# Performance work log

Measured on AMD Instinct MI355X. Metric: run time of the kernel, lower is better.

The kernel has to match this reference:

```python
import jax, jax.numpy as jnp
import numpy as np

B, N, D = 2, 2048, 1024
H = 16
HD = D // H  # 64
SCALE = 8.0 / HD  # muP scale = 0.125
EPS = 1e-5


def setup_inputs() -> dict:
    key = jax.random.key(0)
    ks = jax.random.split(key, 7)
    s = 0.02  # realistic init scale for weights
    return {
        "xq": jax.random.normal(ks[0], (B, N, D), jnp.float32),
        "xk": jax.random.normal(ks[1], (B, N, D), jnp.float32),
        "xv": jax.random.normal(ks[2], (B, N, D), jnp.float32),
        "wq": jax.random.normal(ks[3], (D, D), jnp.float32) * s,
        "wk": jax.random.normal(ks[4], (D, D), jnp.float32) * s,
        "wv": jax.random.normal(ks[5], (D, D), jnp.float32) * s,
        "wproj": jax.random.normal(ks[6], (D, D), jnp.float32) * s,
    }


def _layernorm_noaffine(x):
    # Fp32LayerNorm over last dim, no bias / no affine params
    x32 = x.astype(jnp.float32)
    mu = jnp.mean(x32, axis=-1, keepdims=True)
    var = jnp.mean(jnp.square(x32 - mu), axis=-1, keepdims=True)
    return ((x32 - mu) * jax.lax.rsqrt(var + EPS)).astype(x.dtype)


def _heads(x):
    # [B, N, H*HD] -> [B, H, N, HD]
    b, n, _ = x.shape
    return x.reshape(b, n, H, HD).transpose(0, 2, 1, 3)


def reference(xq, xk, xv, wq, wk, wv, wproj):
    # nn.Linear: y = x @ W^T (no bias)
    q = _heads(xq @ wq.T)
    k = _heads(xk @ wk.T)
    v = _heads(xv @ wv.T)
    q = _layernorm_noaffine(q)
    k = _layernorm_noaffine(k)
    # dense attention (score_mod=None, block_mask=None), muP scale
    scores = jnp.einsum("bhqd,bhkd->bhqk", q, k) * SCALE
    attn = jax.nn.softmax(scores, axis=-1)
    o = jnp.einsum("bhqk,bhkd->bhqd", attn, v)
    o = o.transpose(0, 2, 1, 3).reshape(xq.shape[0], xq.shape[1], D)
    return o @ wproj.T
```

## Files before the change

### kernel.cpp

```cpp
#include <hip/hip_runtime.h>

typedef __bf16 bf16x8 __attribute__((ext_vector_type(8)));
typedef float f32x4 __attribute__((ext_vector_type(4)));
typedef float f32x16 __attribute__((ext_vector_type(16)));
typedef unsigned u32x4 __attribute__((ext_vector_type(4)));

#define DEV __device__ __forceinline__
#define L2E 1.44269504f

DEV unsigned short f2bf(float f) {
  unsigned u = __float_as_uint(f);
  u += 0x7fffu + ((u >> 16) & 1u);
  return (unsigned short)(u >> 16);
}
DEV float bf2f(unsigned short h) { return __uint_as_float(((unsigned)h) << 16); }

DEV void gload16(const void* g, void* l) {
  __builtin_amdgcn_global_load_lds((const __attribute__((address_space(1))) void*)g,
                                   (__attribute__((address_space(3))) void*)l, 16, 0, 0);
}

DEV unsigned cvtpk2(float lo, float hi) {
  unsigned r;
  asm("v_cvt_pk_bf16_f32 %0, %1, %2" : "=v"(r) : "v"(lo), "v"(hi));
  return r;
}
DEV void plswap(unsigned& a, unsigned& b) {
  asm volatile("v_permlane32_swap_b32 %0, %1" : "+v"(a), "+v"(b));
}
DEV float ex2(float x) {
  float r;
  asm("v_exp_f32 %0, %1" : "=v"(r) : "v"(x));
  return r;
}
DEV float max3(float a, float b, float c) {
  float r;
  asm("v_max3_f32 %0, %1, %2, %3" : "=v"(r) : "v"(a), "v"(b), "v"(c));
  return r;
}


__global__ __launch_bounds__(256) void cvt7(const float* xq, const float* xk, const float* xv,
                                            const float* wq, const float* wk, const float* wv,
                                            const float* wp, ushort4* xqb, ushort4* xkb,
                                            ushort4* xvb, ushort4* wqb, ushort4* wkb,
                                            ushort4* wvb, ushort4* wpb, int nx4, int nw4) {
  const int y = blockIdx.y;
  const float4* s;
  ushort4* d;
  int n;
  switch (y) {
    case 0: s = (const float4*)xq; d = xqb; n = nx4; break;
    case 1: s = (const float4*)xk; d = xkb; n = nx4; break;
    case 2: s = (const float4*)xv; d = xvb; n = nx4; break;
    case 3: s = (const float4*)wq; d = wqb; n = nw4; break;
    case 4: s = (const float4*)wk; d = wkb; n = nw4; break;
    case 5: s = (const float4*)wv; d = wvb; n = nw4; break;
    default: s = (const float4*)wp; d = wpb; n = nw4; break;
  }
  for (int i = blockIdx.x * 256 + threadIdx.x; i < n; i += gridDim.x * 256) {
    float4 v = s[i];
    ushort4 o;
    o.x = f2bf(v.x); o.y = f2bf(v.y); o.z = f2bf(v.z); o.w = f2bf(v.w);
    d[i] = o;
  }
}

template <bool SWAP>
DEV void gemm_core(const unsigned short* __restrict__ A, const unsigned short* __restrict__ W,
                   char* sA, char* sB, f32x4 acc[4][4], int bm, int bn, int tid) {
  const int w = tid >> 6, lane = tid & 63;
  const int wm = w >> 1, wn = w & 1;
  const char* aB = (const char*)A + ((size_t)(bm * 128 + (lane >> 3)) << 11) +
                   (((lane & 7) ^ (lane >> 3)) << 4);
  const char* bB = (const char*)W + ((size_t)(bn * 128 + (lane >> 3)) << 11) +
                   (((lane & 7) ^ (lane >> 3)) << 4);
  const int ldsBase = w * 1024;

  for (int kt = 0; kt < 16; ++kt) {
    const int ko = kt * 128;
#pragma unroll
    for (int c = 0; c < 4; ++c) {
      gload16(aB + ((size_t)(c * 32 + w * 8) << 11) + ko, sA + c * 4096 + ldsBase);
      gload16(bB + ((size_t)(c * 32 + w * 8) << 11) + ko, sB + c * 4096 + ldsBase);
    }
    __syncthreads();
#pragma unroll
    for (int kk = 0; kk < 2; ++kk) {
      const int ch = ((kk * 4 + (lane >> 4)) ^ (lane & 7)) << 4;
      bf16x8 aF[4], bF[4];
#pragma unroll
      for (int mi = 0; mi < 4; ++mi)
        aF[mi] = *(const bf16x8*)(sA + (wm * 64 + mi * 16 + (lane & 15)) * 128 + ch);
#pragma unroll
      for (int ni = 0; ni < 4; ++ni)
        bF[ni] = *(const bf16x8*)(sB + (wn * 64 + ni * 16 + (lane & 15)) * 128 + ch);
#pragma unroll
      for (int mi = 0; mi < 4; ++mi)
#pragma unroll
        for (int ni = 0; ni < 4; ++ni)
          acc[mi][ni] = SWAP ? __builtin_amdgcn_mfma_f32_16x16x32_bf16(bF[ni], aF[mi],
                                                                       acc[mi][ni], 0, 0, 0)
                             : __builtin_amdgcn_mfma_f32_16x16x32_bf16(aF[mi], bF[ni],
                                                                       acc[mi][ni], 0, 0, 0);
    }
    __syncthreads();
  }
}

__global__ __launch_bounds__(256, 3) void gemm_qkv(
    const unsigned short* __restrict__ xq, const unsigned short* __restrict__ xk,
    const unsigned short* __restrict__ xv, const unsigned short* __restrict__ wq,
    const unsigned short* __restrict__ wk, const unsigned short* __restrict__ wv,
    unsigned short* __restrict__ qh, unsigned short* __restrict__ kh,
    unsigned short* __restrict__ vt) {
  __shared__ char sA[16384], sB[16384];
  const int z = blockIdx.z;
  const int flat = blockIdx.x + (blockIdx.y << 3);
  const int xcd = flat & 7, ii = flat >> 3;
  const int bm = xcd * 4 + (ii >> 3), bn = ii & 7;
  const int tid = threadIdx.x, w = tid >> 6, lane = tid & 63;
  const int wm = w >> 1, wn = w & 1;

  if (z == 2) {
    f32x4 acc[4][4];
#pragma unroll
    for (int i = 0; i < 4; ++i)
#pragma unroll
      for (int j = 0; j < 4; ++j) acc[i][j] = (f32x4){0.f, 0.f, 0.f, 0.f};
    gemm_core<false>(xv, wv, sA, sB, acc, bm, bn, tid);
    const int hb = bn * 2 + wn;
    const int d = (lane & 15);
    const int g0 = bm * 128 + wm * 64 + ((lane >> 4) << 2);
#pragma unroll
    for (int mi = 0; mi < 4; ++mi) {
      const int g = g0 + mi * 16;
      const int b = g >> 11, n0 = g & 2047, tq = n0 >> 6, nn = n0 & 63;
#pragma unroll
      for (int ni = 0; ni < 4; ++ni) {
        const int dd = d + ni * 16;
        char* dst = (char*)vt + ((size_t)((b * 16 + hb) * 32 + tq) << 13) +
                    (((nn >> 4) * 2 + (dd >> 5)) << 10) + (((nn >> 3) & 1) << 9) +
                    ((dd & 31) << 4) + ((nn & 7) << 1);
        *(uint2*)dst = make_uint2(cvtpk2(acc[mi][ni][0], acc[mi][ni][1]),
                                  cvtpk2(acc[mi][ni][2], acc[mi][ni][3]));
      }
    }
  } else {
    const unsigned short* A = z == 0 ? xq : xk;
    const unsigned short* W = z == 0 ? wq : wk;
    f32x4 acc[4][4];
#pragma unroll
    for (int i = 0; i < 4; ++i)
#pragma unroll
      for (int j = 0; j < 4; ++j) acc[i][j] = (f32x4){0.f, 0.f, 0.f, 0.f};
    gemm_core<true>(A, W, sA, sB, acc, bm, bn, tid);
    unsigned short* dst = z == 0 ? qh : kh;
    const float osc = z == 0 ? 0.125f * L2E : 1.0f;
    const int h = bn * 2 + wn;
    const int hiK = lane >> 5;
    const int low8 = ((lane >> 4) & 1) << 3;
#pragma unroll
    for (int mi = 0; mi < 4; ++mi) {
      float s = 0.f, ss = 0.f;
#pragma unroll
      for (int ni = 0; ni < 4; ++ni)
#pragma unroll
        for (int r = 0; r < 4; ++r) {
          const float v = acc[mi][ni][r];
          s += v;
          ss += v * v;
        }
      s += __shfl_xor(s, 16); ss += __shfl_xor(ss, 16);
      s += __shfl_xor(s, 32); ss += __shfl_xor(ss, 32);
      const float mean = s * 0.015625f;
      const float var = ss * 0.015625f - mean * mean;
      const float rstd = rsqrtf(var + 1e-5f) * osc;
      const float mr = mean * rstd;
      const int g = bm * 128 + wm * 64 + mi * 16 + (lane & 15);
      const int b = g >> 11, n = g & 2047;
      const int bh = b * 16 + h, tq = n >> 6, rr = n & 63;
      char* tbase = (char*)dst + ((size_t)(bh * 32 + tq) << 13);
#pragma unroll
      for (int ni = 0; ni < 4; ++ni) {
        const unsigned u0 = cvtpk2(fmaf(acc[mi][ni][0], rstd, -mr), fmaf(acc[mi][ni][1], rstd, -mr));
        const unsigned u1 = cvtpk2(fmaf(acc[mi][ni][2], rstd, -mr), fmaf(acc[mi][ni][3], rstd, -mr));
        char* p = tbase + ((ni * 2 + (rr >> 5)) << 10) + (hiK << 9) + ((rr & 31) << 4) + low8;
        *(uint2*)p = make_uint2(u0, u1);
      }
    }
  }
}

__global__ __launch_bounds__(256, 3) void gemm_out(const unsigned short* __restrict__ A,
                                                   const unsigned short* __restrict__ Wp,
                                                   float* __restrict__ C) {
  __shared__ char sA[16384], sB[8192];
  const int flat = blockIdx.x + (blockIdx.y << 4);
  const int xcd = flat & 7, ii = flat >> 3;
  const int bm = xcd * 4 + (ii & 3), bn = ii >> 2;
  const int tid = threadIdx.x, w = tid >> 6, lane = tid & 63;
  const int wm = w >> 1, wn = w & 1;
  f32x4 acc[4][2];
#pragma unroll
  for (int i = 0; i < 4; ++i)
#pragma unroll
    for (int j = 0; j < 2; ++j) acc[i][j] = (f32x4){0.f, 0.f, 0.f, 0.f};

  const char* aB = (const char*)A + ((size_t)(bm * 128 + (lane >> 3)) << 11) +
                   (((lane & 7) ^ (lane >> 3)) << 4);
  const char* bB = (const char*)Wp + ((size_t)(bn * 64 + (lane >> 3)) << 11) +
                   (((lane & 7) ^ (lane >> 3)) << 4);
  const int ldsBase = w * 1024;
  for (int kt = 0; kt < 16; ++kt) {
    const int ko = kt * 128;
#pragma unroll
    for (int c = 0; c < 4; ++c)
      gload16(aB + ((size_t)(c * 32 + w * 8) << 11) + ko, sA + c * 4096 + ldsBase);
#pragma unroll
    for (int c = 0; c < 2; ++c)
      gload16(bB + ((size_t)(c * 32 + w * 8) << 11) + ko, sB + c * 4096 + ldsBase);
    __syncthreads();
#pragma unroll
    for (int kk = 0; kk < 2; ++kk) {
      const int ch = ((kk * 4 + (lane >> 4)) ^ (lane & 7)) << 4;
      bf16x8 aF[4], bF[2];
#pragma unroll
      for (int mi = 0; mi < 4; ++mi)
        aF[mi] = *(const bf16x8*)(sA + (wm * 64 + mi * 16 + (lane & 15)) * 128 + ch);
#pragma unroll
      for (int ni = 0; ni < 2; ++ni)
        bF[ni] = *(const bf16x8*)(sB + (wn * 32 + ni * 16 + (lane & 15)) * 128 + ch);
#pragma unroll
      for (int mi = 0; mi < 4; ++mi)
#pragma unroll
        for (int ni = 0; ni < 2; ++ni)
          acc[mi][ni] = __builtin_amdgcn_mfma_f32_16x16x32_bf16(bF[ni], aF[mi], acc[mi][ni], 0, 0, 0);
    }
    __syncthreads();
  }
  const int m0 = bm * 128 + wm * 64 + (lane & 15);
  const int nb = bn * 64 + wn * 32 + ((lane >> 4) << 2);
#pragma unroll
  for (int mi = 0; mi < 4; ++mi)
#pragma unroll
    for (int ni = 0; ni < 2; ++ni) {
      const f32x4 v = acc[mi][ni];
      *(float4*)&C[(size_t)(m0 + mi * 16) * 1024 + nb + ni * 16] =
          make_float4(v[0], v[1], v[2], v[3]);
    }
}

__global__ __launch_bounds__(256, 4) void attn_fused(
    const unsigned short* __restrict__ Qp, const unsigned short* __restrict__ Kp,
    const unsigned short* __restrict__ Vp, unsigned short* __restrict__ Opart,
    float2* __restrict__ ML) {
  const int bid = blockIdx.x;
  const int xcd = bid & 7, idx = bid >> 3;
  const int bh = ((idx & 3) << 3) | xcd;
  const int rest = idx >> 2;
  const int half = rest & 1;
  const int qt = rest >> 1;
  __shared__ char smem[32768];
  const int tid = threadIdx.x, w = tid >> 6, lane = tid & 63;
  const int q5 = lane & 31, hi = lane >> 5;

  const char* qg = (const char*)Qp + ((size_t)(bh * 32 + qt * 2) << 13);
  const char* kg = (const char*)Kp + ((size_t)(bh * 32 + half * 16) << 13);
  const char* vg = (const char*)Vp + ((size_t)(bh * 32 + half * 16) << 13);

#pragma unroll
  for (int t = 0; t < 4; ++t)
    gload16(qg + (w * 4 + t) * 1024 + lane * 16, smem + (w * 4 + t) * 1024);
  __syncthreads();
  bf16x8 qf[4];
  {
    const int qbase = (w >> 1) * 8192 + ((w & 1) << 10);
#pragma unroll
    for (int dc = 0; dc < 4; ++dc)
      qf[dc] = *(const bf16x8*)(smem + qbase + (dc << 11) + lane * 16);
  }
  __syncthreads();

#pragma unroll
  for (int t = 0; t < 2; ++t) {
    gload16(kg + (w * 2 + t) * 1024 + lane * 16, smem + (w * 2 + t) * 1024);
    gload16(vg + (w * 2 + t) * 1024 + lane * 16, smem + 16384 + (w * 2 + t) * 1024);
  }

  const u32x4 onesw = {0x3F803F80u, 0x3F803F80u, 0x3F803F80u, 0x3F803F80u};
  const bf16x8 ones = __builtin_bit_cast(bf16x8, onesw);

  f32x16 o0 = {0,0,0,0,0,0,0,0,0,0,0,0,0,0,0,0};
  f32x16 o1 = {0,0,0,0,0,0,0,0,0,0,0,0,0,0,0,0};
  f32x16 lacc = {0,0,0,0,0,0,0,0,0,0,0,0,0,0,0,0};
  float m = -1e30f;

  for (int kt = 0; kt < 16; ++kt) {
    const int cur = kt & 1;
    const int kOff = cur * 8192;
    const int vOff = 16384 + cur * 8192;
    __syncthreads();
    if (kt < 15) {
      const int kN = (cur ^ 1) * 8192, vN = 16384 + (cur ^ 1) * 8192;
#pragma unroll
      for (int t = 0; t < 2; ++t) {
        gload16(kg + (size_t)(kt + 1) * 8192 + (w * 2 + t) * 1024 + lane * 16,
                smem + kN + (w * 2 + t) * 1024);
        gload16(vg + (size_t)(kt + 1) * 8192 + (w * 2 + t) * 1024 + lane * 16,
                smem + vN + (w * 2 + t) * 1024);
      }
    }
    f32x16 s0 = {0,0,0,0,0,0,0,0,0,0,0,0,0,0,0,0};
    f32x16 s1 = {0,0,0,0,0,0,0,0,0,0,0,0,0,0,0,0};
    __builtin_amdgcn_s_setprio(1);
#pragma unroll
    for (int dc = 0; dc < 4; ++dc) {
      const bf16x8 kf0 = *(const bf16x8*)(smem + kOff + (dc << 11) + lane * 16);
      const bf16x8 kf1 = *(const bf16x8*)(smem + kOff + (dc << 11) + 1024 + lane * 16);
      s0 = __builtin_amdgcn_mfma_f32_32x32x16_bf16(kf0, qf[dc], s0, 0, 0, 0);
      s1 = __builtin_amdgcn_mfma_f32_32x32x16_bf16(kf1, qf[dc], s1, 0, 0, 0);
    }
    __builtin_amdgcn_s_setprio(0);
    float tt[12];
#pragma unroll
    for (int r = 0; r < 10; ++r) {
      const float a = (3 * r) < 16 ? s0[(3 * r) & 15] : s1[(3 * r) & 15];
      const float b = (3 * r + 1) < 16 ? s0[(3 * r + 1) & 15] : s1[(3 * r + 1) & 15];
      const float c = (3 * r + 2) < 16 ? s0[(3 * r + 2) & 15] : s1[(3 * r + 2) & 15];
      tt[r] = max3(a, b, c);
    }
    tt[10] = s1[14]; tt[11] = s1[15];
    tt[0] = max3(tt[0], tt[1], tt[2]);
    tt[1] = max3(tt[3], tt[4], tt[5]);
    tt[2] = max3(tt[6], tt[7], tt[8]);
    tt[3] = max3(tt[9], tt[10], tt[11]);
    const float loc = fmaxf(max3(tt[0], tt[1], tt[2]), tt[3]);
    const float mx = fmaxf(loc, __shfl_xor(loc, 32));
    if (__any(mx > m + 8.f)) {
      const float mn = fmaxf(m, mx);
      const float corr = ex2(m - mn);
      lacc[0] *= corr;
#pragma unroll
      for (int r = 0; r < 16; ++r) { o0[r] *= corr; o1[r] *= corr; }
      m = mn;
    }
    const float nm = -m;
    unsigned pk[4][4];
#define DO_CHUNK(c, SV, B)                                      \
  {                                                             \
    float p0 = ex2(SV[B + 0] + nm);                             \
    float p1 = ex2(SV[B + 1] + nm);                             \
    float p2 = ex2(SV[B + 2] + nm);                             \
    float p3 = ex2(SV[B + 3] + nm);                             \
    float p4 = ex2(SV[B + 4] + nm);                             \
    float p5 = ex2(SV[B + 5] + nm);                             \
    float p6 = ex2(SV[B + 6] + nm);                             \
    float p7 = ex2(SV[B + 7] + nm);                             \
    unsigned a0 = cvtpk2(p0, p1), a1 = cvtpk2(p2, p3);          \
    unsigned b0 = cvtpk2(p4, p5), b1 = cvtpk2(p6, p7);          \
    plswap(a0, b0);                                             \
    plswap(a1, b1);                                             \
    pk[c][0] = a0; pk[c][1] = a1; pk[c][2] = b0; pk[c][3] = b1; \
  }
    DO_CHUNK(0, s0, 0)
    DO_CHUNK(1, s0, 8)
    DO_CHUNK(2, s1, 0)
    DO_CHUNK(3, s1, 8)
#undef DO_CHUNK
    __builtin_amdgcn_s_setprio(1);
#pragma unroll
    for (int kk = 0; kk < 4; ++kk) {
      const bf16x8 vf0 = *(const bf16x8*)(smem + vOff + (kk << 11) + lane * 16);
      const bf16x8 vf1 = *(const bf16x8*)(smem + vOff + (kk << 11) + 1024 + lane * 16);
      const u32x4 pw = {pk[kk][0], pk[kk][1], pk[kk][2], pk[kk][3]};
      const bf16x8 pb = __builtin_bit_cast(bf16x8, pw);
      o0 = __builtin_amdgcn_mfma_f32_32x32x16_bf16(vf0, pb, o0, 0, 0, 0);
      o1 = __builtin_amdgcn_mfma_f32_32x32x16_bf16(vf1, pb, o1, 0, 0, 0);
      lacc = __builtin_amdgcn_mfma_f32_32x32x16_bf16(ones, pb, lacc, 0, 0, 0);
    }
    __builtin_amdgcn_s_setprio(0);
  }

  const float l = lacc[0];
  const float invl = 1.f / l;
  const int q = qt * 128 + w * 32 + q5;
  const size_t prow = (size_t)(half * 32 + bh) * 2048 + q;
  unsigned short* ob = Opart + prow * 64;
#pragma unroll
  for (int g = 0; g < 4; ++g) {
    unsigned d0 = cvtpk2(o0[4 * g + 0] * invl, o0[4 * g + 1] * invl);
    unsigned d1 = cvtpk2(o0[4 * g + 2] * invl, o0[4 * g + 3] * invl);
    *(uint2*)(ob + 8 * g + 4 * hi) = make_uint2(d0, d1);
    unsigned e0 = cvtpk2(o1[4 * g + 0] * invl, o1[4 * g + 1] * invl);
    unsigned e1 = cvtpk2(o1[4 * g + 2] * invl, o1[4 * g + 3] * invl);
    *(uint2*)(ob + 32 + 8 * g + 4 * hi) = make_uint2(e0, e1);
  }
  if (hi == 0) ML[prow] = make_float2(m, l);
}

__global__ __launch_bounds__(256) void attn_merge(const unsigned short* __restrict__ Op,
                                                  const float2* __restrict__ ML,
                                                  unsigned short* __restrict__ O) {
  const int gid = blockIdx.x * 256 + threadIdx.x;
  const int row = gid >> 3, sub = gid & 7;
  float2 ml[2];
  float mm = -1e30f;
#pragma unroll
  for (int p = 0; p < 2; ++p) {
    ml[p] = ML[p * 65536 + row];
    mm = fmaxf(mm, ml[p].x);
  }
  float wgt[2], wsum = 0.f;
#pragma unroll
  for (int p = 0; p < 2; ++p) {
    wgt[p] = ml[p].y * ex2(ml[p].x - mm);
    wsum += wgt[p];
  }
  const float inv = 1.f / wsum;
  float r[8] = {0.f, 0.f, 0.f, 0.f, 0.f, 0.f, 0.f, 0.f};
#pragma unroll
  for (int p = 0; p < 2; ++p) {
    const uint4 a = *(const uint4*)(Op + ((size_t)(p * 65536) + row) * 64 + sub * 8);
    const unsigned av[4] = {a.x, a.y, a.z, a.w};
#pragma unroll
    for (int j = 0; j < 4; ++j) {
      r[2 * j] += wgt[p] * bf2f((unsigned short)(av[j] & 0xffff));
      r[2 * j + 1] += wgt[p] * bf2f((unsigned short)(av[j] >> 16));
    }
  }
  unsigned ov[4];
#pragma unroll
  for (int j = 0; j < 4; ++j)
    ov[j] = cvtpk2(r[2 * j] * inv, r[2 * j + 1] * inv);
  const int bh = row >> 11, q = row & 2047, bb = bh >> 4, h = bh & 15;
  *(uint4*)(O + ((size_t)(bb * 2048 + q) * 1024 + h * 64 + sub * 8)) =
      make_uint4(ov[0], ov[1], ov[2], ov[3]);
}

extern "C" void kernel_launch(void* const* d_in, const int* in_sizes, int n_in,
                              void* d_out, int out_size, void* d_ws, size_t ws_size,
                              hipStream_t stream) {
  const float* xq = (const float*)d_in[0];
  const float* xk = (const float*)d_in[1];
  const float* xv = (const float*)d_in[2];
  const float* wq = (const float*)d_in[3];
  const float* wk = (const float*)d_in[4];
  const float* wv = (const float*)d_in[5];
  const float* wp = (const float*)d_in[6];

  const size_t NX = 4194304;
  const size_t NW = 1048576;
  unsigned short* base = (unsigned short*)d_ws;
  unsigned short* xqb = base;
  unsigned short* xkb = base + NX;
  unsigned short* xvb = base + 2 * NX;
  unsigned short* wqb = base + 3 * NX;
  unsigned short* wkb = wqb + NW;
  unsigned short* wvb = wkb + NW;
  unsigned short* wpb = base + 3 * NX + 4 * NW;
  unsigned short* qh = wpb + NW;
  unsigned short* kh = qh + NX;
  unsigned short* vt = kh + NX;
  unsigned short* obf = vt + NX;
  float2* ml = (float2*)(obf + NX);
  unsigned short* opart = base;

  cvt7<<<dim3(512, 7), 256, 0, stream>>>(xq, xk, xv, wq, wk, wv, wp, (ushort4*)xqb,
                                         (ushort4*)xkb, (ushort4*)xvb, (ushort4*)wqb,
                                         (ushort4*)wkb, (ushort4*)wvb, (ushort4*)wpb,
                                         (int)(NX / 4), (int)(NW / 4));

  gemm_qkv<<<dim3(8, 32, 3), 256, 0, stream>>>(xqb, xkb, xvb, wqb, wkb, wvb, qh, kh, vt);

  attn_fused<<<1024, 256, 0, stream>>>(qh, kh, vt, opart, ml);
  attn_merge<<<2048, 256, 0, stream>>>(opart, ml, obf);

  gemm_out<<<dim3(16, 32), 256, 0, stream>>>(obf, wpb, (float*)d_out);
}
```

Baseline: 122.9 us.

## Triple-buffer K/V tiles in attention with prefetch depth two and vmcnt waits

Moves the attention kernel's K/V shared-memory staging from double to triple buffering. Tiles are prefetched two iterations ahead, and a partial s_waitcnt vmcnt(4) plus a raw barrier replaces the per-iteration __syncthreads. The aim is to hide more global-load latency behind the MFMA work. The cost is 48KB of LDS per block, with launch bounds lowered to 3 blocks per CU, which may reduce occupancy and latency hiding across waves.

```diff
diff --git a/kernel.cpp b/kernel.cpp
--- a/kernel.cpp
+++ b/kernel.cpp
@@ -251,7 +251,7 @@
     }
 }
 
-__global__ __launch_bounds__(256, 4) void attn_fused(
+__global__ __launch_bounds__(256, 3) void attn_fused(
     const unsigned short* __restrict__ Qp, const unsigned short* __restrict__ Kp,
     const unsigned short* __restrict__ Vp, unsigned short* __restrict__ Opart,
     float2* __restrict__ ML) {
@@ -261,7 +261,7 @@
   const int rest = idx >> 2;
   const int half = rest & 1;
   const int qt = rest >> 1;
-  __shared__ char smem[32768];
+  __shared__ char smem[49152];
   const int tid = threadIdx.x, w = tid >> 6, lane = tid & 63;
   const int q5 = lane & 31, hi = lane >> 5;
 
@@ -283,10 +283,14 @@
   __syncthreads();
 
 #pragma unroll
-  for (int t = 0; t < 2; ++t) {
-    gload16(kg + (w * 2 + t) * 1024 + lane * 16, smem + (w * 2 + t) * 1024);
-    gload16(vg + (w * 2 + t) * 1024 + lane * 16, smem + 16384 + (w * 2 + t) * 1024);
-  }
+  for (int tt = 0; tt < 2; ++tt)
+#pragma unroll
+    for (int t = 0; t < 2; ++t) {
+      gload16(kg + (size_t)tt * 8192 + (w * 2 + t) * 1024 + lane * 16,
+              smem + tt * 8192 + (w * 2 + t) * 1024);
+      gload16(vg + (size_t)tt * 8192 + (w * 2 + t) * 1024 + lane * 16,
+              smem + 24576 + tt * 8192 + (w * 2 + t) * 1024);
+    }
 
   const u32x4 onesw = {0x3F803F80u, 0x3F803F80u, 0x3F803F80u, 0x3F803F80u};
   const bf16x8 ones = __builtin_bit_cast(bf16x8, onesw);
@@ -296,57 +300,60 @@
   f32x16 lacc = {0,0,0,0,0,0,0,0,0,0,0,0,0,0,0,0};
   float m = -1e30f;
 
-  for (int kt = 0; kt < 16; ++kt) {
-    const int cur = kt & 1;
-    const int kOff = cur * 8192;
-    const int vOff = 16384 + cur * 8192;
-    __syncthreads();
-    if (kt < 15) {
-      const int kN = (cur ^ 1) * 8192, vN = 16384 + (cur ^ 1) * 8192;
-#pragma unroll
-      for (int t = 0; t < 2; ++t) {
-        gload16(kg + (size_t)(kt + 1) * 8192 + (w * 2 + t) * 1024 + lane * 16,
-                smem + kN + (w * 2 + t) * 1024);
-        gload16(vg + (size_t)(kt + 1) * 8192 + (w * 2 + t) * 1024 + lane * 16,
-                smem + vN + (w * 2 + t) * 1024);
-      }
-    }
-    f32x16 s0 = {0,0,0,0,0,0,0,0,0,0,0,0,0,0,0,0};
-    f32x16 s1 = {0,0,0,0,0,0,0,0,0,0,0,0,0,0,0,0};
-    __builtin_amdgcn_s_setprio(1);
-#pragma unroll
-    for (int dc = 0; dc < 4; ++dc) {
-      const bf16x8 kf0 = *(const bf16x8*)(smem + kOff + (dc << 11) + lane * 16);
-      const bf16x8 kf1 = *(const bf16x8*)(smem + kOff + (dc << 11) + 1024 + lane * 16);
-      s0 = __builtin_amdgcn_mfma_f32_32x32x16_bf16(kf0, qf[dc], s0, 0, 0, 0);
-      s1 = __builtin_amdgcn_mfma_f32_32x32x16_bf16(kf1, qf[dc], s1, 0, 0, 0);
-    }
-    __builtin_amdgcn_s_setprio(0);
-    float tt[12];
-#pragma unroll
-    for (int r = 0; r < 10; ++r) {
-      const float a = (3 * r) < 16 ? s0[(3 * r) & 15] : s1[(3 * r) & 15];
-      const float b = (3 * r + 1) < 16 ? s0[(3 * r + 1) & 15] : s1[(3 * r + 1) & 15];
-      const float c = (3 * r + 2) < 16 ? s0[(3 * r + 2) & 15] : s1[(3 * r + 2) & 15];
-      tt[r] = max3(a, b, c);
-    }
-    tt[10] = s1[14]; tt[11] = s1[15];
-    tt[0] = max3(tt[0], tt[1], tt[2]);
-    tt[1] = max3(tt[3], tt[4], tt[5]);
-    tt[2] = max3(tt[6], tt[7], tt[8]);
-    tt[3] = max3(tt[9], tt[10], tt[11]);
-    const float loc = fmaxf(max3(tt[0], tt[1], tt[2]), tt[3]);
-    const float mx = fmaxf(loc, __shfl_xor(loc, 32));
-    if (__any(mx > m + 8.f)) {
-      const float mn = fmaxf(m, mx);
-      const float corr = ex2(m - mn);
-      lacc[0] *= corr;
-#pragma unroll
-      for (int r = 0; r < 16; ++r) { o0[r] *= corr; o1[r] *= corr; }
-      m = mn;
-    }
-    const float nm = -m;
-    unsigned pk[4][4];
+#define ATTN_TILE(kOff, vOff)                                                     \
+  {                                                                               \
+    f32x16 s0 = {0,0,0,0,0,0,0,0,0,0,0,0,0,0,0,0};                                \
+    f32x16 s1 = {0,0,0,0,0,0,0,0,0,0,0,0,0,0,0,0};                                \
+    __builtin_amdgcn_s_setprio(1);                                                \
+    _Pragma("unroll") for (int dc = 0; dc < 4; ++dc) {                            \
+      const bf16x8 kf0 = *(const bf16x8*)(smem + (kOff) + (dc << 11) + lane * 16);\
+      const bf16x8 kf1 =                                                          \
+          *(const bf16x8*)(smem + (kOff) + (dc << 11) + 1024 + lane * 16);        \
+      s0 = __builtin_amdgcn_mfma_f32_32x32x16_bf16(kf0, qf[dc], s0, 0, 0, 0);     \
+      s1 = __builtin_amdgcn_mfma_f32_32x32x16_bf16(kf1, qf[dc], s1, 0, 0, 0);     \
+    }                                                                             \
+    __builtin_amdgcn_s_setprio(0);                                                \
+    float tt[12];                                                                 \
+    _Pragma("unroll") for (int r = 0; r < 10; ++r) {                              \
+      const float a = (3 * r) < 16 ? s0[(3 * r) & 15] : s1[(3 * r) & 15];         \
+      const float b = (3 * r + 1) < 16 ? s0[(3 * r + 1) & 15] : s1[(3 * r + 1) & 15]; \
+      const float c = (3 * r + 2) < 16 ? s0[(3 * r + 2) & 15] : s1[(3 * r + 2) & 15]; \
+      tt[r] = max3(a, b, c);                                                      \
+    }                                                                             \
+    tt[10] = s1[14]; tt[11] = s1[15];                                             \
+    tt[0] = max3(tt[0], tt[1], tt[2]);                                            \
+    tt[1] = max3(tt[3], tt[4], tt[5]);                                            \
+    tt[2] = max3(tt[6], tt[7], tt[8]);                                            \
+    tt[3] = max3(tt[9], tt[10], tt[11]);                                          \
+    const float loc = fmaxf(max3(tt[0], tt[1], tt[2]), tt[3]);                    \
+    const float mx = fmaxf(loc, __shfl_xor(loc, 32));                             \
+    if (__any(mx > m + 8.f)) {                                                    \
+      const float mn = fmaxf(m, mx);                                              \
+      const float corr = ex2(m - mn);                                             \
+      lacc[0] *= corr;                                                            \
+      _Pragma("unroll") for (int r = 0; r < 16; ++r) { o0[r] *= corr; o1[r] *= corr; } \
+      m = mn;                                                                     \
+    }                                                                             \
+    const float nm = -m;                                                          \
+    unsigned pk[4][4];                                                            \
+    DO_CHUNK(0, s0, 0)                                                            \
+    DO_CHUNK(1, s0, 8)                                                            \
+    DO_CHUNK(2, s1, 0)                                                            \
+    DO_CHUNK(3, s1, 8)                                                            \
+    __builtin_amdgcn_s_setprio(1);                                                \
+    _Pragma("unroll") for (int kk = 0; kk < 4; ++kk) {                            \
+      const bf16x8 vf0 = *(const bf16x8*)(smem + (vOff) + (kk << 11) + lane * 16);\
+      const bf16x8 vf1 =                                                          \
+          *(const bf16x8*)(smem + (vOff) + (kk << 11) + 1024 + lane * 16);        \
+      const u32x4 pw = {pk[kk][0], pk[kk][1], pk[kk][2], pk[kk][3]};              \
+      const bf16x8 pb = __builtin_bit_cast(bf16x8, pw);                           \
+      o0 = __builtin_amdgcn_mfma_f32_32x32x16_bf16(vf0, pb, o0, 0, 0, 0);         \
+      o1 = __builtin_amdgcn_mfma_f32_32x32x16_bf16(vf1, pb, o1, 0, 0, 0);         \
+      lacc = __builtin_amdgcn_mfma_f32_32x32x16_bf16(ones, pb, lacc, 0, 0, 0);    \
+    }                                                                             \
+    __builtin_amdgcn_s_setprio(0);                                                \
+  }
+
 #define DO_CHUNK(c, SV, B)                                      \
   {                                                             \
     float p0 = ex2(SV[B + 0] + nm);                             \
@@ -363,24 +370,36 @@
     plswap(a1, b1);                                             \
     pk[c][0] = a0; pk[c][1] = a1; pk[c][2] = b0; pk[c][3] = b1; \
   }
-    DO_CHUNK(0, s0, 0)
-    DO_CHUNK(1, s0, 8)
-    DO_CHUNK(2, s1, 0)
-    DO_CHUNK(3, s1, 8)
+
+  int cb = 0;
+  for (int kt = 0; kt < 15; ++kt) {
+    asm volatile("s_waitcnt vmcnt(4)" ::: "memory");
+    __builtin_amdgcn_s_barrier();
+    __builtin_amdgcn_sched_barrier(0);
+    if (kt < 14) {
+      const int pb = cb == 0 ? 2 : cb - 1;
+      const char* kgp = kg + ((size_t)(kt + 2) << 13);
+      const char* vgp = vg + ((size_t)(kt + 2) << 13);
+#pragma unroll
+      for (int t = 0; t < 2; ++t) {
+        gload16(kgp + (w * 2 + t) * 1024 + lane * 16, smem + pb * 8192 + (w * 2 + t) * 1024);
+        gload16(vgp + (w * 2 + t) * 1024 + lane * 16,
+                smem + 24576 + pb * 8192 + (w * 2 + t) * 1024);
+      }
+    }
+    const int kOff = cb * 8192, vOff = 24576 + cb * 8192;
+    ATTN_TILE(kOff, vOff)
+    cb = cb == 2 ? 0 : cb + 1;
+  }
+  {
+    asm volatile("s_waitcnt vmcnt(0)" ::: "memory");
+    __builtin_amdgcn_s_barrier();
+    __builtin_amdgcn_sched_barrier(0);
+    const int kOff = cb * 8192, vOff = 24576 + cb * 8192;
+    ATTN_TILE(kOff, vOff)
+  }
 #undef DO_CHUNK
-    __builtin_amdgcn_s_setprio(1);
-#pragma unroll
-    for (int kk = 0; kk < 4; ++kk) {
-      const bf16x8 vf0 = *(const bf16x8*)(smem + vOff + (kk << 11) + lane * 16);
-      const bf16x8 vf1 = *(const bf16x8*)(smem + vOff + (kk << 11) + 1024 + lane * 16);
-      const u32x4 pw = {pk[kk][0], pk[kk][1], pk[kk][2], pk[kk][3]};
-      const bf16x8 pb = __builtin_bit_cast(bf16x8, pw);
-      o0 = __builtin_amdgcn_mfma_f32_32x32x16_bf16(vf0, pb, o0, 0, 0, 0);
-      o1 = __builtin_amdgcn_mfma_f32_32x32x16_bf16(vf1, pb, o1, 0, 0, 0);
-      lacc = __builtin_amdgcn_mfma_f32_32x32x16_bf16(ones, pb, lacc, 0, 0, 0);
-    }
-    __builtin_amdgcn_s_setprio(0);
-  }
+#undef ATTN_TILE
 
   const float l = lacc[0];
   const float invl = 1.f / l;
```

After: 126.1 us. 2.7% more time.

## Fuse split-KV attention merge into output projection GEMM A-tile load

Applied to the files above, without the earlier changes.

Removes the separate attn_merge kernel and instead combines the two partial attention outputs, weighted by their stored max and sum statistics, while staging the A tile of the output GEMM into shared memory. This saves one launch and one round trip of the merged bf16 activation through global memory. In exchange the GEMM's A loads become synchronous register loads plus ALU work instead of asynchronous global-to-LDS copies. Each merged row is also recomputed by every N-block of the GEMM (16 times), which adds redundant global reads of the partials.

```diff
diff --git a/kernel.cpp b/kernel.cpp
--- a/kernel.cpp
+++ b/kernel.cpp
@@ -192,7 +192,8 @@
   }
 }
 
-__global__ __launch_bounds__(256, 3) void gemm_out(const unsigned short* __restrict__ A,
+__global__ __launch_bounds__(256, 3) void gemm_out(const unsigned short* __restrict__ Op,
+                                                   const float2* __restrict__ ML,
                                                    const unsigned short* __restrict__ Wp,
                                                    float* __restrict__ C) {
   __shared__ char sA[16384], sB[8192];
@@ -207,19 +208,45 @@
 #pragma unroll
     for (int j = 0; j < 2; ++j) acc[i][j] = (f32x4){0.f, 0.f, 0.f, 0.f};
 
-  const char* aB = (const char*)A + ((size_t)(bm * 128 + (lane >> 3)) << 11) +
-                   (((lane & 7) ^ (lane >> 3)) << 4);
   const char* bB = (const char*)Wp + ((size_t)(bn * 64 + (lane >> 3)) << 11) +
                    (((lane & 7) ^ (lane >> 3)) << 4);
   const int ldsBase = w * 1024;
+  const int rsub = lane >> 3;
+  const int ch8 = (lane & 7) ^ rsub;
+  const int d0 = ch8 * 8;
+
   for (int kt = 0; kt < 16; ++kt) {
     const int ko = kt * 128;
 #pragma unroll
-    for (int c = 0; c < 4; ++c)
-      gload16(aB + ((size_t)(c * 32 + w * 8) << 11) + ko, sA + c * 4096 + ldsBase);
-#pragma unroll
     for (int c = 0; c < 2; ++c)
       gload16(bB + ((size_t)(c * 32 + w * 8) << 11) + ko, sB + c * 4096 + ldsBase);
+#pragma unroll
+    for (int c = 0; c < 4; ++c) {
+      const int grow = bm * 128 + c * 32 + w * 8 + rsub;
+      const int b = grow >> 11, q = grow & 2047;
+      const size_t pr0 = (size_t)(b * 16 + kt) * 2048 + q;
+      const size_t pr1 = pr0 + 65536;
+      const uint4 pa = *(const uint4*)(Op + pr0 * 64 + d0);
+      const uint4 pb = *(const uint4*)(Op + pr1 * 64 + d0);
+      const float2 ml0 = ML[pr0], ml1 = ML[pr1];
+      const float mm = fmaxf(ml0.x, ml1.x);
+      float w0 = ml0.y * ex2(ml0.x - mm);
+      float w1 = ml1.y * ex2(ml1.x - mm);
+      const float inv = 1.f / (w0 + w1);
+      w0 *= inv; w1 *= inv;
+      const unsigned av[4] = {pa.x, pa.y, pa.z, pa.w};
+      const unsigned bv[4] = {pb.x, pb.y, pb.z, pb.w};
+      unsigned ov[4];
+#pragma unroll
+      for (int j = 0; j < 4; ++j) {
+        const float r0 = w0 * bf2f((unsigned short)(av[j] & 0xffff)) +
+                         w1 * bf2f((unsigned short)(bv[j] & 0xffff));
+        const float r1 = w0 * bf2f((unsigned short)(av[j] >> 16)) +
+                         w1 * bf2f((unsigned short)(bv[j] >> 16));
+        ov[j] = cvtpk2(r0, r1);
+      }
+      *(u32x4*)(sA + c * 4096 + ldsBase + lane * 16) = (u32x4){ov[0], ov[1], ov[2], ov[3]};
+    }
     __syncthreads();
 #pragma unroll
     for (int kk = 0; kk < 2; ++kk) {
@@ -399,45 +426,6 @@
   if (hi == 0) ML[prow] = make_float2(m, l);
 }
 
-__global__ __launch_bounds__(256) void attn_merge(const unsigned short* __restrict__ Op,
-                                                  const float2* __restrict__ ML,
-                                                  unsigned short* __restrict__ O) {
-  const int gid = blockIdx.x * 256 + threadIdx.x;
-  const int row = gid >> 3, sub = gid & 7;
-  float2 ml[2];
-  float mm = -1e30f;
-#pragma unroll
-  for (int p = 0; p < 2; ++p) {
-    ml[p] = ML[p * 65536 + row];
-    mm = fmaxf(mm, ml[p].x);
-  }
-  float wgt[2], wsum = 0.f;
-#pragma unroll
-  for (int p = 0; p < 2; ++p) {
-    wgt[p] = ml[p].y * ex2(ml[p].x - mm);
-    wsum += wgt[p];
-  }
-  const float inv = 1.f / wsum;
-  float r[8] = {0.f, 0.f, 0.f, 0.f, 0.f, 0.f, 0.f, 0.f};
-#pragma unroll
-  for (int p = 0; p < 2; ++p) {
-    const uint4 a = *(const uint4*)(Op + ((size_t)(p * 65536) + row) * 64 + sub * 8);
-    const unsigned av[4] = {a.x, a.y, a.z, a.w};
-#pragma unroll
-    for (int j = 0; j < 4; ++j) {
-      r[2 * j] += wgt[p] * bf2f((unsigned short)(av[j] & 0xffff));
-      r[2 * j + 1] += wgt[p] * bf2f((unsigned short)(av[j] >> 16));
-    }
-  }
-  unsigned ov[4];
-#pragma unroll
-  for (int j = 0; j < 4; ++j)
-    ov[j] = cvtpk2(r[2 * j] * inv, r[2 * j + 1] * inv);
-  const int bh = row >> 11, q = row & 2047, bb = bh >> 4, h = bh & 15;
-  *(uint4*)(O + ((size_t)(bb * 2048 + q) * 1024 + h * 64 + sub * 8)) =
-      make_uint4(ov[0], ov[1], ov[2], ov[3]);
-}
-
 extern "C" void kernel_launch(void* const* d_in, const int* in_sizes, int n_in,
                               void* d_out, int out_size, void* d_ws, size_t ws_size,
                               hipStream_t stream) {
@@ -474,7 +462,6 @@
   gemm_qkv<<<dim3(8, 32, 3), 256, 0, stream>>>(xqb, xkb, xvb, wqb, wkb, wvb, qh, kh, vt);
 
   attn_fused<<<1024, 256, 0, stream>>>(qh, kh, vt, opart, ml);
-  attn_merge<<<2048, 256, 0, stream>>>(opart, ml, obf);
-
-  gemm_out<<<dim3(16, 32), 256, 0, stream>>>(obf, wpb, (float*)d_out);
-}
+
+  gemm_out<<<dim3(16, 32), 256, 0, stream>>>(opart, ml, wpb, (float*)d_out);
+}
```

New measurement: 142.0 us. 15.6% more time.
